# Performance work log

Hardware: AMD Instinct MI355X
Metric: run time of the kernel (lower is better)

The kernel has to match this reference:

```python
import jax, jax.numpy as jnp
import numpy as np

KROT = 8        # number of pairwise-rotation layers (hard-coded in Rotation)
GROUP = 128     # rotation group size (hard-coded)
QGS = 128       # quantization group size (hard-coded in RotateLinearAWQMarlinInt4)


def setup_inputs() -> dict:
    rng = np.random.default_rng(0)
    M, K, N = 32, 8192, 28672
    G = K // QGS  # 64 quant groups
    shifts = np.arange(8, dtype=np.uint32) * 4
    # activations
    x = jnp.asarray(rng.standard_normal((M, K)), dtype=jnp.float16)
    # int4 weights packed 8-per-int32 along the out dim (nibble j of word n -> column n*8+j)
    nib = rng.integers(0, 16, size=(K, N // 8, 8), dtype=np.uint32)
    qweight = jnp.asarray((nib << shifts).sum(-1, dtype=np.uint32).view(np.int32))  # (K, N//8)
    znib = rng.integers(0, 16, size=(G, N // 8, 8), dtype=np.uint32)
    qzeros = jnp.asarray((znib << shifts).sum(-1, dtype=np.uint32).view(np.int32))  # (G, N//8)
    scales = jnp.asarray(rng.uniform(0.001, 0.01, (G, N)), dtype=jnp.float16)
    bias = jnp.asarray(rng.standard_normal(N) * 0.01, dtype=jnp.float16)
    # rotation params: per-layer angles over all K//2 pairs; one local permutation of
    # 0..127 per layer, shared across all K//GROUP groups (as in Rotation.__init__)
    theta = jnp.asarray(rng.uniform(-0.2, 0.2, (KROT, K // 2)), dtype=jnp.float16)
    pairs = jnp.asarray(np.stack([rng.permutation(GROUP) for _ in range(KROT)]).astype(np.int32))  # (KROT, 128)
    channel_scales = jnp.asarray(rng.uniform(0.5, 2.0, (1, K)), dtype=jnp.float16)
    return dict(x=x, qweight=qweight, qzeros=qzeros, scales=scales, bias=bias,
                theta=theta, pairs=pairs, channel_scales=channel_scales)


def _rotate(x, pairs, theta, channel_scales):
    # x: (M, K). Apply KROT layers of Givens rotations on channel pairs within each
    # 128-wide group, then per-channel scaling.
    M, K = x.shape
    ng = K // GROUP
    xg = x.reshape(M, ng, GROUP)
    for k in range(KROT):
        p = pairs[k]                      # (128,) local permutation
        i, j = p[0::2], p[1::2]           # (64,) disjoint index sets
        th = theta[k].reshape(ng, GROUP // 2).astype(jnp.float32)  # (ng, 64) per-group angles
        c = jnp.cos(th).astype(x.dtype)
        s = jnp.sin(th).astype(x.dtype)
        xi = xg[:, :, i]
        xj = xg[:, :, j]
        xg = xg.at[:, :, i].set(c * xi - s * xj)
        xg = xg.at[:, :, j].set(s * xi + c * xj)
    return xg.reshape(M, K) * channel_scales


def _dequant(qweight, qzeros, scales):
    # unpack 8 uint4 nibbles per int32 along the out dim; dequant per quant group
    K = qweight.shape[0]
    shifts = jnp.arange(8, dtype=jnp.int32) * 4
    w = ((qweight[:, :, None] >> shifts) & 0xF).reshape(K, -1)       # (K, N) ints 0..15
    z = ((qzeros[:, :, None] >> shifts) & 0xF).reshape(qzeros.shape[0], -1)  # (G, N)
    zf = jnp.repeat(z.astype(scales.dtype), QGS, axis=0)             # (K, N)
    sf = jnp.repeat(scales, QGS, axis=0)                             # (K, N)
    return (w.astype(scales.dtype) - zf) * sf


def reference(x, qweight, qzeros, scales, bias, theta, pairs, channel_scales):
    xr = _rotate(x, pairs, theta, channel_scales)   # (M, K)
    W = _dequant(qweight, qzeros, scales)           # (K, N)
    return xr @ W + bias
```

## Files before the change

### kernel.cpp

```cpp
#include <hip/hip_runtime.h>
#include <hip/hip_bf16.h>

using uint32   = unsigned int;
using ushort_t = unsigned short;
using short8   = __attribute__((ext_vector_type(8))) short;
using uint4v   = __attribute__((ext_vector_type(4))) uint32;
using float4v  = __attribute__((ext_vector_type(4))) float;
using floatx16 = __attribute__((ext_vector_type(16))) float;

#define M_DIM 32
#define K_DIM 8192
#define N_DIM 28672
#define QROW  (N_DIM/8)
#define KSPLIT 8
#define BN    128
#define NB    (N_DIM/BN)
#define CH    128
#define NCH   8
#define TCOLS (BN/8)
#define TSTRIDE 132

__device__ ushort_t g_xr2[M_DIM * K_DIM];
__device__ float    g_S[64 * M_DIM];

__device__ __forceinline__ float bf2f(ushort_t u){
  unsigned int v = ((unsigned int)u) << 16;
  return __builtin_bit_cast(float, v);
}
__device__ __forceinline__ ushort_t f2bf(float f){
  return __builtin_bit_cast(ushort_t, __float2bfloat16(f));
}

#define LDS_BARRIER() do {                                   \
  asm volatile("s_waitcnt lgkmcnt(0)" ::: "memory");         \
  __builtin_amdgcn_s_barrier();                              \
  asm volatile("" ::: "memory");                             \
} while (0)

__global__ __launch_bounds__(256) void prep_kernel(
    const float* __restrict__ x, const float* __restrict__ theta,
    const int* __restrict__ pairs, const float* __restrict__ cs,
    const float* __restrict__ bias, float* __restrict__ out)
{
  if (blockIdx.x >= 512){
    const int b  = blockIdx.x - 512;
    const int n  = (b % (N_DIM/256))*256 + threadIdx.x;
    const int m0 = (b / (N_DIM/256))*8;
    const float bv = bias[n];
    #pragma unroll
    for (int m = 0; m < 8; ++m) out[(size_t)(m0+m)*N_DIM + n] = bv;
    return;
  }
  __shared__ float xb[4][128];
  const int u    = threadIdx.x >> 6;
  const int lane = threadIdx.x & 63;
  const int id   = blockIdx.x * 4 + u;
  const int m    = id >> 6;
  const int g    = id & 63;
  const float* xp = x + m*K_DIM + g*128;
  int   ip[8], jp[8];
  float cv[8], sv[8];
  #pragma unroll
  for (int k = 0; k < 8; ++k){
    ip[k] = pairs[k*128 + 2*lane];
    jp[k] = pairs[k*128 + 2*lane + 1];
    const float th = theta[k*(K_DIM/2) + g*64 + lane];
    cv[k] = cosf(th); sv[k] = sinf(th);
  }
  xb[u][lane]    = xp[lane];
  xb[u][lane+64] = xp[lane+64];
  #pragma unroll
  for (int k = 0; k < 8; ++k){
    __syncthreads();
    const float xi = xb[u][ip[k]], xj = xb[u][jp[k]];
    xb[u][ip[k]] = cv[k]*xi - sv[k]*xj;
    xb[u][jp[k]] = sv[k]*xi + cv[k]*xj;
  }
  __syncthreads();
  const int base = g*128;
  const int k0 = base + lane, k1 = base + lane + 64;
  const ushort_t b0 = f2bf(xb[u][lane]    * cs[k0]);
  const ushort_t b1 = f2bf(xb[u][lane+64] * cs[k1]);
  g_xr2[(((size_t)(k0>>3))*32 + m)*8 + (k0&7)] = b0;
  g_xr2[(((size_t)(k1>>3))*32 + m)*8 + (k1&7)] = b1;
  float sum = bf2f(b0) + bf2f(b1);
  #pragma unroll
  for (int d = 32; d > 0; d >>= 1) sum += __shfl_xor(sum, d, 64);
  if (lane == 0) g_S[g*M_DIM + m] = sum;
}

__global__ __launch_bounds__(256, 4) void gemm_kernel(
    const uint32* __restrict__ qw, const uint32* __restrict__ qz,
    const float* __restrict__ scales, float* __restrict__ out)
{
  __shared__ uint32 T[2][TCOLS*TSTRIDE];
  const int bid  = blockIdx.x;
  const int ks   = bid & (KSPLIT-1);
  const int nb   = bid >> 3;
  const int tid  = threadIdx.x;
  const int w    = tid >> 6;
  const int lane = tid & 63;
  const int l31  = lane & 31;
  const int koct = lane >> 5;
  const int n0   = nb * BN;
  const int n    = n0 + w*32 + l31;
  const uint32 sh = (uint32)((l31 & 7)*4);
  const int col  = w*4 + (l31 >> 3);
  const int k0   = ks * (NCH*CH);

  const int brow = tid >> 2;
  const int bcq  = tid & 3;
  const uint32* bbase = qw + (size_t)(k0 + brow)*QROW + (n0>>3) + bcq*4;
  const ushort_t* abase = g_xr2 + (size_t)k0*32;

  uint4v bv0[4], bv1[4];
  #pragma unroll
  for (int c = 0; c < 4; ++c){
    const uint32* bb = bbase + (size_t)c*CH*QROW;
    bv0[c] = *(const uint4v*)(bb);
    bv1[c] = *(const uint4v*)(bb + (size_t)64*QROW);
  }

  float accT[16];
  #pragma unroll
  for (int r = 0; r < 16; ++r) accT[r] = 0.f;

  #pragma unroll
  for (int j = 0; j < 4; ++j){
    const int mj = (j + bcq) & 3;
    T[0][(bcq*4 + mj)*TSTRIDE + brow]      = bv0[0][mj];
    T[0][(bcq*4 + mj)*TSTRIDE + brow + 64] = bv1[0][mj];
  }
  {
    const uint32* bb = bbase + (size_t)4*CH*QROW;
    bv0[0] = *(const uint4v*)(bb);
    bv1[0] = *(const uint4v*)(bb + (size_t)64*QROW);
  }
  LDS_BARRIER();

  #pragma unroll
  for (int c = 0; c < NCH; ++c){
    const int cb = c & 1, nx = cb ^ 1;
    const float  s  = scales[(size_t)(ks*NCH + c)*N_DIM + n];
    const uint32 zq = qz[(size_t)(ks*NCH + c)*QROW + (n>>3)];
    if (c + 1 < NCH){
      #pragma unroll
      for (int j = 0; j < 4; ++j){
        const int mj = (j + bcq) & 3;
        T[nx][(bcq*4 + mj)*TSTRIDE + brow]      = bv0[(c+1)&3][mj];
        T[nx][(bcq*4 + mj)*TSTRIDE + brow + 64] = bv1[(c+1)&3][mj];
      }
    }
    if (c + 5 < NCH){
      const uint32* bb = bbase + (size_t)(c+5)*CH*QROW;
      bv0[(c+1)&3] = *(const uint4v*)(bb);
      bv1[(c+1)&3] = *(const uint4v*)(bb + (size_t)64*QROW);
    }

    const ushort_t* ab = abase + (size_t)c*CH*32;

    floatx16 acc;
    #pragma unroll
    for (int r = 0; r < 16; ++r) acc[r] = 0.f;

    #pragma unroll
    for (int kh = 0; kh < 2; ++kh){
      short8 av[4];
      #pragma unroll
      for (int i = 0; i < 4; ++i){
        const int kk = kh*4 + i;
        av[i] = *(const short8*)(ab + ((kk*2 + koct)*32 + l31)*8);
      }
      #pragma unroll
      for (int i = 0; i < 4; ++i){
        const int kk = kh*4 + i;
        const uint32* tp = &T[cb][col*TSTRIDE + kk*16 + koct*8];
        const uint4v p0 = *(const uint4v*)(tp);
        const uint4v p1 = *(const uint4v*)(tp + 4);
        uint4v bp;
        bp.x = ((p0.x >> sh) & 15u) | (((p0.y >> sh) & 15u) << 16) | 0x43004300u;
        bp.y = ((p0.z >> sh) & 15u) | (((p0.w >> sh) & 15u) << 16) | 0x43004300u;
        bp.z = ((p1.x >> sh) & 15u) | (((p1.y >> sh) & 15u) << 16) | 0x43004300u;
        bp.w = ((p1.z >> sh) & 15u) | (((p1.w >> sh) & 15u) << 16) | 0x43004300u;
        acc = __builtin_amdgcn_mfma_f32_32x32x16_bf16(
                  av[i], __builtin_bit_cast(short8, bp), acc, 0, 0, 0);
      }
    }
    const float t = s * (float)(128u + ((zq >> sh) & 15u));
    const float* Sg = &g_S[(size_t)(ks*NCH + c)*M_DIM];
    float4v Sv[4];
    #pragma unroll
    for (int q = 0; q < 4; ++q)
      Sv[q] = *(const float4v*)(Sg + q*8 + 4*koct);
    #pragma unroll
    for (int r = 0; r < 16; ++r){
      accT[r] = fmaf(s, acc[r], accT[r]);
      accT[r] = fmaf(-t, Sv[r >> 2][r & 3], accT[r]);
    }
    if (c + 1 < NCH) LDS_BARRIER();
  }
  #pragma unroll
  for (int r = 0; r < 16; ++r){
    const int row = (r & 3) + 8*(r >> 2) + 4*koct;
    atomicAdd(out + (size_t)row*N_DIM + n, accT[r]);
  }
}

extern "C" void kernel_launch(void* const* d_in, const int* in_sizes, int n_in,
                              void* d_out, int out_size, void* d_ws, size_t ws_size,
                              hipStream_t stream)
{
  const float*  x      = (const float*)d_in[0];
  const uint32* qw     = (const uint32*)d_in[1];
  const uint32* qz     = (const uint32*)d_in[2];
  const float*  scales = (const float*)d_in[3];
  const float*  bias   = (const float*)d_in[4];
  const float*  theta  = (const float*)d_in[5];
  const int*    pairs  = (const int*)d_in[6];
  const float*  cs     = (const float*)d_in[7];
  float* out = (float*)d_out;

  prep_kernel<<<dim3(512 + (N_DIM/256)*4), dim3(256), 0, stream>>>(
      x, theta, pairs, cs, bias, out);
  gemm_kernel<<<dim3(NB*KSPLIT), dim3(256), 0, stream>>>(qw, qz, scales, out);
}
```

Before: 222.3 us.

## Stage int4 weight tiles via direct global-to-LDS loads with triple buffering

New measurement: 230.1 us. +3.5%, slower.

```diff
diff --git a/kernel.cpp b/kernel.cpp
--- a/kernel.cpp
+++ b/kernel.cpp
@@ -17,8 +17,9 @@
 #define NB    (N_DIM/BN)
 #define CH    128
 #define NCH   8
-#define TCOLS (BN/8)
-#define TSTRIDE 132
+
+typedef __attribute__((address_space(3))) uint32 lds_u32;
+typedef const __attribute__((address_space(1))) uint32 glb_u32;
 
 __device__ ushort_t g_xr2[M_DIM * K_DIM];
 __device__ float    g_S[64 * M_DIM];
@@ -30,12 +31,6 @@
 __device__ __forceinline__ ushort_t f2bf(float f){
   return __builtin_bit_cast(ushort_t, __float2bfloat16(f));
 }
-
-#define LDS_BARRIER() do {                                   \
-  asm volatile("s_waitcnt lgkmcnt(0)" ::: "memory");         \
-  __builtin_amdgcn_s_barrier();                              \
-  asm volatile("" ::: "memory");                             \
-} while (0)
 
 __global__ __launch_bounds__(256) void prep_kernel(
     const float* __restrict__ x, const float* __restrict__ theta,
@@ -93,7 +88,7 @@
     const uint32* __restrict__ qw, const uint32* __restrict__ qz,
     const float* __restrict__ scales, float* __restrict__ out)
 {
-  __shared__ uint32 T[2][TCOLS*TSTRIDE];
+  __shared__ uint32 T[3][CH*16];
   const int bid  = blockIdx.x;
   const int ks   = bid & (KSPLIT-1);
   const int nb   = bid >> 3;
@@ -108,96 +103,78 @@
   const int col  = w*4 + (l31 >> 3);
   const int k0   = ks * (NCH*CH);
 
-  const int brow = tid >> 2;
-  const int bcq  = tid & 3;
-  const uint32* bbase = qw + (size_t)(k0 + brow)*QROW + (n0>>3) + bcq*4;
+  const int srow = tid >> 2;
+  const int scq  = (tid & 3)*4;
+  const uint32* sbase = qw + (size_t)(k0 + srow)*QROW + (n0>>3) + scq;
   const ushort_t* abase = g_xr2 + (size_t)k0*32;
 
-  uint4v bv0[4], bv1[4];
-  #pragma unroll
-  for (int c = 0; c < 4; ++c){
-    const uint32* bb = bbase + (size_t)c*CH*QROW;
-    bv0[c] = *(const uint4v*)(bb);
-    bv1[c] = *(const uint4v*)(bb + (size_t)64*QROW);
-  }
+  auto stage = [&](int c, int b){
+    #pragma unroll
+    for (int q = 0; q < 2; ++q){
+      const uint32* gp = sbase + (size_t)(c*CH + q*64)*QROW;
+      lds_u32* lp = (lds_u32*)&T[b][q*1024 + w*256];
+      __builtin_amdgcn_global_load_lds((glb_u32*)gp, lp, 16, 0, 0);
+    }
+  };
 
   float accT[16];
   #pragma unroll
   for (int r = 0; r < 16; ++r) accT[r] = 0.f;
 
-  #pragma unroll
-  for (int j = 0; j < 4; ++j){
-    const int mj = (j + bcq) & 3;
-    T[0][(bcq*4 + mj)*TSTRIDE + brow]      = bv0[0][mj];
-    T[0][(bcq*4 + mj)*TSTRIDE + brow + 64] = bv1[0][mj];
-  }
-  {
-    const uint32* bb = bbase + (size_t)4*CH*QROW;
-    bv0[0] = *(const uint4v*)(bb);
-    bv1[0] = *(const uint4v*)(bb + (size_t)64*QROW);
-  }
-  LDS_BARRIER();
+  stage(0, 0);
+  stage(1, 1);
+  asm volatile("s_waitcnt vmcnt(2)" ::: "memory");
+  __builtin_amdgcn_s_barrier();
+  asm volatile("" ::: "memory");
 
   #pragma unroll
   for (int c = 0; c < NCH; ++c){
-    const int cb = c & 1, nx = cb ^ 1;
+    const int cb = c % 3;
     const float  s  = scales[(size_t)(ks*NCH + c)*N_DIM + n];
     const uint32 zq = qz[(size_t)(ks*NCH + c)*QROW + (n>>3)];
-    if (c + 1 < NCH){
-      #pragma unroll
-      for (int j = 0; j < 4; ++j){
-        const int mj = (j + bcq) & 3;
-        T[nx][(bcq*4 + mj)*TSTRIDE + brow]      = bv0[(c+1)&3][mj];
-        T[nx][(bcq*4 + mj)*TSTRIDE + brow + 64] = bv1[(c+1)&3][mj];
-      }
-    }
-    if (c + 5 < NCH){
-      const uint32* bb = bbase + (size_t)(c+5)*CH*QROW;
-      bv0[(c+1)&3] = *(const uint4v*)(bb);
-      bv1[(c+1)&3] = *(const uint4v*)(bb + (size_t)64*QROW);
-    }
-
-    const ushort_t* ab = abase + (size_t)c*CH*32;
-
-    floatx16 acc;
-    #pragma unroll
-    for (int r = 0; r < 16; ++r) acc[r] = 0.f;
-
-    #pragma unroll
-    for (int kh = 0; kh < 2; ++kh){
-      short8 av[4];
-      #pragma unroll
-      for (int i = 0; i < 4; ++i){
-        const int kk = kh*4 + i;
-        av[i] = *(const short8*)(ab + ((kk*2 + koct)*32 + l31)*8);
-      }
-      #pragma unroll
-      for (int i = 0; i < 4; ++i){
-        const int kk = kh*4 + i;
-        const uint32* tp = &T[cb][col*TSTRIDE + kk*16 + koct*8];
-        const uint4v p0 = *(const uint4v*)(tp);
-        const uint4v p1 = *(const uint4v*)(tp + 4);
-        uint4v bp;
-        bp.x = ((p0.x >> sh) & 15u) | (((p0.y >> sh) & 15u) << 16) | 0x43004300u;
-        bp.y = ((p0.z >> sh) & 15u) | (((p0.w >> sh) & 15u) << 16) | 0x43004300u;
-        bp.z = ((p1.x >> sh) & 15u) | (((p1.y >> sh) & 15u) << 16) | 0x43004300u;
-        bp.w = ((p1.z >> sh) & 15u) | (((p1.w >> sh) & 15u) << 16) | 0x43004300u;
-        acc = __builtin_amdgcn_mfma_f32_32x32x16_bf16(
-                  av[i], __builtin_bit_cast(short8, bp), acc, 0, 0, 0);
-      }
-    }
-    const float t = s * (float)(128u + ((zq >> sh) & 15u));
     const float* Sg = &g_S[(size_t)(ks*NCH + c)*M_DIM];
     float4v Sv[4];
     #pragma unroll
     for (int q = 0; q < 4; ++q)
       Sv[q] = *(const float4v*)(Sg + q*8 + 4*koct);
+    const ushort_t* ab = abase + (size_t)c*CH*32;
+    short8 av[8];
+    #pragma unroll
+    for (int i = 0; i < 8; ++i)
+      av[i] = *(const short8*)(ab + ((i*2 + koct)*32 + l31)*8);
+    if (c + 2 < NCH) stage(c + 2, (c + 2) % 3);
+
+    floatx16 acc;
+    #pragma unroll
+    for (int r = 0; r < 16; ++r) acc[r] = 0.f;
+
+    const uint32* Tc = &T[cb][0];
+    #pragma unroll
+    for (int kk = 0; kk < 8; ++kk){
+      const int rb = kk*16 + koct*8;
+      uint32 p[8];
+      #pragma unroll
+      for (int j = 0; j < 8; ++j) p[j] = Tc[(rb + j)*16 + col];
+      uint4v bp;
+      bp.x = ((p[0] >> sh) & 15u) | (((p[1] >> sh) & 15u) << 16) | 0x43004300u;
+      bp.y = ((p[2] >> sh) & 15u) | (((p[3] >> sh) & 15u) << 16) | 0x43004300u;
+      bp.z = ((p[4] >> sh) & 15u) | (((p[5] >> sh) & 15u) << 16) | 0x43004300u;
+      bp.w = ((p[6] >> sh) & 15u) | (((p[7] >> sh) & 15u) << 16) | 0x43004300u;
+      acc = __builtin_amdgcn_mfma_f32_32x32x16_bf16(
+                av[kk], __builtin_bit_cast(short8, bp), acc, 0, 0, 0);
+    }
+    const float t = s * (float)(128u + ((zq >> sh) & 15u));
     #pragma unroll
     for (int r = 0; r < 16; ++r){
       accT[r] = fmaf(s, acc[r], accT[r]);
       accT[r] = fmaf(-t, Sv[r >> 2][r & 3], accT[r]);
     }
-    if (c + 1 < NCH) LDS_BARRIER();
+    if (c + 1 < NCH){
+      asm volatile("s_waitcnt vmcnt(2)" ::: "memory");
+      asm volatile("s_waitcnt lgkmcnt(0)" ::: "memory");
+      __builtin_amdgcn_s_barrier();
+      asm volatile("" ::: "memory");
+    }
   }
   #pragma unroll
   for (int r = 0; r < 16; ++r){
```
